# Kernel tuning notes

Measured on AMD Instinct MI355X. Metric: run time of the kernel, lower is better.

The kernel has to match this reference:

```python
import jax, jax.numpy as jnp
import numpy as np

BN_EPS = 1e-5


def ball_query(pos, radius, k):
    """PointNet++-style ball query: for each point, the first k point indices
    (in index order) whose distance < radius; shorter lists are padded with the
    first valid index (self is always valid since dist=0). pos: (b,n,3).
    Returns idx: (b,n,k) int32."""
    b, n, _ = pos.shape
    sq = jnp.sum(pos * pos, axis=-1)                       # (b,n)
    d2 = sq[:, :, None] + sq[:, None, :] - 2.0 * jnp.einsum('bnc,bmc->bnm', pos, pos)
    mask = d2 < radius * radius                            # (b,n,n)
    cand = jnp.where(mask, jnp.arange(n, dtype=jnp.int32)[None, None, :], jnp.int32(n))
    # smallest-k indices in ascending order == first-k valid in index order
    neg_top, _ = jax.lax.top_k(-cand, k)                   # (b,n,k)
    idx = -neg_top
    first = idx[..., :1]
    idx = jnp.where(idx == n, first, idx)                  # pad with first neighbor
    return idx


def reference(pos, x, w1, gamma, beta, w2, b2, radius, k):
    pos = jax.lax.stop_gradient(pos)
    idx = ball_query(pos, radius, k)                       # (b,n,k)
    grouped = jax.vmap(lambda p, i: p[i])(pos, idx)        # (b,n,k,3)
    rel = grouped - pos[:, :, None, :]                     # center-subtract
    # 1x1 conv (3->3, no bias)
    h = jnp.einsum('bnkc,dc->bnkd', rel, w1)
    # BatchNorm2d (training-mode batch stats over b,k,n per channel)
    mean = jnp.mean(h, axis=(0, 1, 2))
    var = jnp.mean((h - mean) ** 2, axis=(0, 1, 2))
    h = (h - mean) * jax.lax.rsqrt(var + BN_EPS) * gamma + beta
    h = jax.nn.relu(h)
    # 1x1 conv (3->out_channel) + bias
    pe = jnp.einsum('bnkd,ed->bnke', h, w2) + b2           # (b,n,k,C)
    pe = jnp.max(pe, axis=2)                               # max over k neighbors
    return x + pe


def setup_inputs() -> dict:
    key = jax.random.key(0)
    ks = jax.random.split(key, 5)
    b, n, c, kk = 2, 8192, 64, 32
    pos = jax.random.uniform(ks[0], (b, n, 3), dtype=jnp.float32)
    x = jax.random.normal(ks[1], (b, n, c), dtype=jnp.float32)
    w1 = jax.random.normal(ks[2], (3, 3), dtype=jnp.float32) * 0.5
    gamma = jnp.ones((3,), dtype=jnp.float32)
    beta = jnp.zeros((3,), dtype=jnp.float32)
    w2 = jax.random.normal(ks[3], (c, 3), dtype=jnp.float32) * 0.5
    b2 = jnp.zeros((c,), dtype=jnp.float32)
    radius = jnp.float32(0.1)
    return {"pos": pos, "x": x, "w1": w1, "gamma": gamma, "beta": beta,
            "w2": w2, "b2": b2, "radius": radius, "k": kk}
```

## Files before the change

kernel.cpp:

```cpp
#include <hip/hip_runtime.h>
#include <math.h>

#define NPTS   8192
#define NBATCH 2
#define NQ     (NPTS * NBATCH)
#define KNB    32
#define CFEAT  64
#define BN_EPS 1e-5f

#define MAXC     1000
#define CSTR     1024
#define CAP_HIT  128

#define QBK2  16
#define NBLK2 (NQ / QBK2)

#define QBK3  16
#define NBLK3 (NQ / QBK3)

#define WS_H     0
#define WS_PART  (WS_H + NQ * 3 * KNB)
#define WS_STATS (WS_PART + 6 * NBLK2)
#define WS_CS    (WS_STATS + 8)
#define WS_BIN   (WS_CS + 2 * CSTR)

__device__ __forceinline__ int grid_from_r(double rd) {
    int G = (int)(1.0 / rd);
    if (G < 1) G = 1;
    while (G > 1 && 1.0 / (double)G < rd) --G;
    if (G > 10) G = 10;
    return G;
}

__device__ __forceinline__ int mbcnt64(unsigned long long m) {
    return (int)__builtin_amdgcn_mbcnt_hi((unsigned)(m >> 32),
             __builtin_amdgcn_mbcnt_lo((unsigned)m, 0u));
}

__device__ __forceinline__ int cell_of(float v, float Gf, int G) {
    int c = (int)(v * Gf);
    return c > G - 1 ? G - 1 : c;
}

__global__ __launch_bounds__(1024) void kBin(
    const float* __restrict__ pos, const float* __restrict__ radius,
    float* __restrict__ ws)
{
    __shared__ int hist[MAXC];
    __shared__ int cur[MAXC];
    __shared__ int wtot[16];

    const int tid = threadIdx.x, lane = tid & 63, wave = tid >> 6;
    const int batch = blockIdx.x;

    const float* bpos = pos + (size_t)batch * NPTS * 3;
    const double rd = (double)radius[0];
    const int G = grid_from_r(rd);
    const float Gf = (float)G;
    const int NC = G * G * G;

    for (int c = tid; c < NC; c += 1024) hist[c] = 0;
    __syncthreads();

    for (int p = tid; p < NPTS; p += 1024) {
        const float* pp = bpos + (size_t)p * 3;
        int c = (cell_of(pp[2], Gf, G) * G + cell_of(pp[1], Gf, G)) * G
                + cell_of(pp[0], Gf, G);
        atomicAdd(&hist[c], 1);
    }
    __syncthreads();

    int v = (tid < NC) ? hist[tid] : 0;
    int incl = v;
#pragma unroll
    for (int off = 1; off < 64; off <<= 1) {
        int t = __shfl_up(incl, off);
        if (lane >= off) incl += t;
    }
    if (lane == 63) wtot[wave] = incl;
    __syncthreads();
    int base = 0;
#pragma unroll
    for (int w = 0; w < 16; ++w) base += (w < wave) ? wtot[w] : 0;
    const int excl = base + incl - v;
    int* cs = (int*)ws + WS_CS + batch * CSTR;
    if (tid < NC) { cs[tid] = excl; cur[tid] = excl; }
    if (tid == 0) cs[NC] = NPTS;
    __syncthreads();

    float4* bin = (float4*)(ws + WS_BIN) + (size_t)batch * NPTS;
    for (int p = tid; p < NPTS; p += 1024) {
        const float* pp = bpos + (size_t)p * 3;
        float x = pp[0], y = pp[1], z = pp[2];
        int c = (cell_of(z, Gf, G) * G + cell_of(y, Gf, G)) * G
                + cell_of(x, Gf, G);
        int slot = atomicAdd(&cur[c], 1);
        bin[slot] = make_float4(x, y, z, __int_as_float(p));
    }
}

__global__ __launch_bounds__(1024) void k2_query(
    const float* __restrict__ pos, const float* __restrict__ w1,
    const float* __restrict__ radius, float* __restrict__ ws)
{
    __shared__ int   hitl[QBK2][CAP_HIT];
    __shared__ int   seli[QBK2][KNB];
    __shared__ float sred[QBK2][6];

    const int tid = threadIdx.x, lane = tid & 63, wave = tid >> 6;
    const int qbase = blockIdx.x * QBK2;
    const int batch = qbase / NPTS;
    const float* bpos = pos + (size_t)batch * NPTS * 3;
    const double rd  = (double)radius[0];
    const double r2d = rd * rd;
    const int G = grid_from_r(rd);
    const float Gf = (float)G;
    const int* cs = (const int*)ws + WS_CS + batch * CSTR;
    const float4* bin = (const float4*)(ws + WS_BIN) + (size_t)batch * NPTS;

    const int qg = qbase + wave;
    const int ql = qg - batch * NPTS;
    const float qx = bpos[ql * 3], qy = bpos[ql * 3 + 1], qz = bpos[ql * 3 + 2];
    const double qxd = (double)qx, qyd = (double)qy, qzd = (double)qz;
    const double qsd = fma(qzd, qzd, fma(qyd, qyd, qxd * qxd));
    const int cx = cell_of(qx, Gf, G);
    const int cy = cell_of(qy, Gf, G);
    const int cz = cell_of(qz, Gf, G);
    const int cx0 = max(cx - 1, 0), cx1 = min(cx + 1, G - 1);

    int rs0[9], rpref[10];
    int tot = 0;
#pragma unroll
    for (int r = 0; r < 9; ++r) {
        const int ny = cy + (r % 3) - 1;
        const int nz = cz + (r / 3) - 1;
        int s0 = 0, len = 0;
        if (ny >= 0 && ny < G && nz >= 0 && nz < G) {
            const int cb = (nz * G + ny) * G;
            s0  = cs[cb + cx0];
            len = cs[cb + cx1 + 1] - s0;
        }
        rs0[r] = s0; rpref[r] = tot; tot += len;
    }
    rpref[9] = tot;

    int hc = 0;
    for (int b0 = 0; b0 < tot; b0 += 64) {
        const int flat = b0 + lane;
        const bool act = flat < tot;
        int ss = flat + (rs0[0] - rpref[0]);
#pragma unroll
        for (int i = 1; i < 9; ++i)
            ss += (flat >= rpref[i]) ? ((rs0[i] - rpref[i]) -
                                        (rs0[i - 1] - rpref[i - 1])) : 0;
        float4 P = bin[act ? ss : 0];
        double xj = (double)P.x, yj = (double)P.y, zj = (double)P.z;
        double sqj = fma(zj, zj, fma(yj, yj, xj * xj));
        double dot = fma(zj, qzd, fma(yj, qyd, xj * qxd));
        double dd  = (qsd + sqj) - 2.0 * dot;
        bool in = act && (dd < r2d);
        unsigned long long bal = __ballot(in);
        if (in) {
            int p2 = hc + mbcnt64(bal);
            if (p2 < CAP_HIT) hitl[wave][p2] = __float_as_int(P.w);
        }
        hc += (int)__popcll(bal);
    }
    if (hc > CAP_HIT) hc = CAP_HIT;

    if (hc <= KNB) {
        int v = (lane < hc) ? hitl[wave][lane] : 0x7FFFFFFF;
        int mn = v;
#pragma unroll
        for (int off = 32; off; off >>= 1) mn = min(mn, __shfl_xor(mn, off));
        if (lane < KNB) seli[wave][lane] = (lane < hc) ? v : mn;
    } else {
        int a = (lane < hc) ? hitl[wave][lane] : 0x7FFFFFFF;
        int b = (64 + lane < hc) ? hitl[wave][64 + lane] : 0x7FFFFFFF;
        int lo = 0, hi = NPTS - 1;
        while (lo < hi) {
            int mid = (lo + hi) >> 1;
            int c1 = (int)__popcll(__ballot(a <= mid)) +
                     (int)__popcll(__ballot(b <= mid));
            if (c1 >= KNB) hi = mid; else lo = mid + 1;
        }
        const int t = lo;
        unsigned long long ba = __ballot(a <= t);
        unsigned long long bb = __ballot(b <= t);
        int na = (int)__popcll(ba);
        if (a <= t) seli[wave][mbcnt64(ba)] = a;
        if (b <= t) seli[wave][na + mbcnt64(bb)] = b;
    }

    float w1r[9];
#pragma unroll
    for (int i = 0; i < 9; ++i) w1r[i] = w1[i];

    float ls0 = 0.f, ls1 = 0.f, ls2 = 0.f;
    float lq0 = 0.f, lq1 = 0.f, lq2 = 0.f;
    if (lane < KNB) {
        int j = seli[wave][lane];
        const float* pj = bpos + (size_t)j * 3;
        float rx = __fsub_rn(pj[0], qx);
        float ry = __fsub_rn(pj[1], qy);
        float rz = __fsub_rn(pj[2], qz);
        float h0 = fmaf(rz, w1r[2], fmaf(ry, w1r[1], __fmul_rn(rx, w1r[0])));
        float h1 = fmaf(rz, w1r[5], fmaf(ry, w1r[4], __fmul_rn(rx, w1r[3])));
        float h2 = fmaf(rz, w1r[8], fmaf(ry, w1r[7], __fmul_rn(rx, w1r[6])));
        float* hout = ws + WS_H + (size_t)qg * 3 * KNB;
        hout[0 * KNB + lane] = h0;
        hout[1 * KNB + lane] = h1;
        hout[2 * KNB + lane] = h2;
        ls0 = h0; ls1 = h1; ls2 = h2;
        lq0 = h0 * h0; lq1 = h1 * h1; lq2 = h2 * h2;
    }

#pragma unroll
    for (int m = 1; m < 64; m <<= 1) {
        ls0 += __shfl_xor(ls0, m); ls1 += __shfl_xor(ls1, m); ls2 += __shfl_xor(ls2, m);
        lq0 += __shfl_xor(lq0, m); lq1 += __shfl_xor(lq1, m); lq2 += __shfl_xor(lq2, m);
    }
    if (lane == 0) {
        sred[wave][0] = ls0; sred[wave][1] = ls1; sred[wave][2] = ls2;
        sred[wave][3] = lq0; sred[wave][4] = lq1; sred[wave][5] = lq2;
    }
    __syncthreads();
    if (tid < 6) {
        float s = 0.f;
#pragma unroll
        for (int w = 0; w < QBK2; ++w) s += sred[w][tid];
        ws[WS_PART + tid * NBLK2 + blockIdx.x] = s;
    }
}

__global__ __launch_bounds__(1024) void k2b_stats(float* __restrict__ ws)
{
    __shared__ float wred[16][6];
    const int tid = threadIdx.x, lane = tid & 63, wave = tid >> 6;

#pragma unroll
    for (int c = 0; c < 6; ++c) {
        float s = ws[WS_PART + c * NBLK2 + tid];
#pragma unroll
        for (int m = 1; m < 64; m <<= 1) s += __shfl_xor(s, m);
        if (lane == 0) wred[wave][c] = s;
    }
    __syncthreads();
    if (tid < 3) {
        const double N = (double)((long long)NQ * KNB);
        double s = 0.0, sq = 0.0;
#pragma unroll
        for (int w = 0; w < 16; ++w) { s += wred[w][tid]; sq += wred[w][3 + tid]; }
        double mean = s / N;
        double var  = sq / N - mean * mean;
        ws[WS_STATS + tid]     = (float)mean;
        ws[WS_STATS + 3 + tid] = (float)(1.0 / sqrt(var + (double)BN_EPS));
    }
}

__global__ __launch_bounds__(256) void k3_mlp(
    const float* __restrict__ ws, const float* __restrict__ gamma,
    const float* __restrict__ beta, const float* __restrict__ w2,
    const float* __restrict__ b2, const float* __restrict__ x,
    float* __restrict__ out)
{
    __shared__ float gl[QBK3 * 96];

    const int tid = threadIdx.x;
    const float m0 = ws[WS_STATS + 0], m1 = ws[WS_STATS + 1], m2 = ws[WS_STATS + 2];
    const float i0 = ws[WS_STATS + 3], i1 = ws[WS_STATS + 4], i2 = ws[WS_STATS + 5];
    const float g0 = gamma[0], g1 = gamma[1], g2 = gamma[2];
    const float b0 = beta[0],  b1 = beta[1],  b2c = beta[2];

    const int qbase = blockIdx.x * QBK3;
    const float* hin = ws + WS_H + (size_t)qbase * 96;

#pragma unroll
    for (int r = 0; r < 6; ++r) {
        const int idx = r * 256 + tid;
        const int c = (idx % 96) >> 5;
        float h = hin[idx];
        float mm = c == 0 ? m0 : (c == 1 ? m1 : m2);
        float ii = c == 0 ? i0 : (c == 1 ? i1 : i2);
        float gg = c == 0 ? g0 : (c == 1 ? g1 : g2);
        float bb = c == 0 ? b0 : (c == 1 ? b1 : b2c);
        float n = __fadd_rn(__fmul_rn(__fmul_rn(__fsub_rn(h, mm), ii), gg), bb);
        gl[idx] = fmaxf(n, 0.0f);
    }
    __syncthreads();

    const int ch = tid & 63;
    const int qh = tid >> 6;
    const float w20 = w2[ch * 3 + 0];
    const float w21 = w2[ch * 3 + 1];
    const float w22 = w2[ch * 3 + 2];
    const float bias = b2[ch];

#pragma unroll
    for (int r = 0; r < 4; ++r) {
        const int q = r * 4 + qh;
        const float* gq = &gl[q * 96];
        float m = -INFINITY;
#pragma unroll 4
        for (int kk = 0; kk < KNB; ++kk) {
            float ga = gq[kk], gb = gq[32 + kk], gc = gq[64 + kk];
            float pe = __fadd_rn(fmaf(gc, w22, fmaf(gb, w21, __fmul_rn(ga, w20))), bias);
            m = fmaxf(m, pe);
        }
        const size_t o = (size_t)(qbase + q) * CFEAT + ch;
        out[o] = __fadd_rn(x[o], m);
    }
}

extern "C" void kernel_launch(void* const* d_in, const int* in_sizes, int n_in,
                              void* d_out, int out_size, void* d_ws, size_t ws_size,
                              hipStream_t stream) {
    (void)in_sizes; (void)n_in; (void)out_size; (void)ws_size;
    const float* pos    = (const float*)d_in[0];
    const float* x      = (const float*)d_in[1];
    const float* w1     = (const float*)d_in[2];
    const float* gamma  = (const float*)d_in[3];
    const float* beta   = (const float*)d_in[4];
    const float* w2     = (const float*)d_in[5];
    const float* b2     = (const float*)d_in[6];
    const float* radius = (const float*)d_in[7];
    float* out = (float*)d_out;
    float* ws  = (float*)d_ws;

    hipLaunchKernelGGL(kBin,      dim3(NBATCH), dim3(1024), 0, stream, pos, radius, ws);
    hipLaunchKernelGGL(k2_query,  dim3(NBLK2),  dim3(1024), 0, stream, pos, w1, radius, ws);
    hipLaunchKernelGGL(k2b_stats, dim3(1),      dim3(1024), 0, stream, ws);
    hipLaunchKernelGGL(k3_mlp,    dim3(NBLK3),  dim3(256),  0, stream,
                       ws, gamma, beta, w2, b2, x, out);
}
```

Measured before the change: 56.87 us.

## Replace stats reduction kernel with fixed-point atomics and prefetch candidate loads

Drops the single-block BN statistics kernel. Each query block now adds its partial sums into 64-bit fixed-point accumulators with atomics, and the MLP kernel derives mean and inverse std from those accumulators itself, which removes one launch and one dependency gap. The candidate scan in the query kernel also software-pipelines the bin loads by prefetching the next 64-wide chunk while testing the current one. The fixed-point scaling adds a small quantization error to the statistics, and the accumulators are zeroed inside kBin, which relies on kernels running in stream order.

```diff
diff --git a/kernel.cpp b/kernel.cpp
--- a/kernel.cpp
+++ b/kernel.cpp
@@ -11,6 +11,7 @@
 #define MAXC     1000
 #define CSTR     1024
 #define CAP_HIT  128
+#define ACC_SCALE 16777216.0
 
 #define QBK2  16
 #define NBLK2 (NQ / QBK2)
@@ -19,9 +20,8 @@
 #define NBLK3 (NQ / QBK3)
 
 #define WS_H     0
-#define WS_PART  (WS_H + NQ * 3 * KNB)
-#define WS_STATS (WS_PART + 6 * NBLK2)
-#define WS_CS    (WS_STATS + 8)
+#define WS_ACC   (WS_H + NQ * 3 * KNB)
+#define WS_CS    (WS_ACC + 12)
 #define WS_BIN   (WS_CS + 2 * CSTR)
 
 __device__ __forceinline__ int grid_from_r(double rd) {
@@ -52,6 +52,8 @@
 
     const int tid = threadIdx.x, lane = tid & 63, wave = tid >> 6;
     const int batch = blockIdx.x;
+    if (batch == 0 && tid < 6)
+        ((long long*)(ws + WS_ACC))[tid] = 0LL;
 
     const float* bpos = pos + (size_t)batch * NPTS * 3;
     const double rd = (double)radius[0];
@@ -143,18 +145,34 @@
         rs0[r] = s0; rpref[r] = tot; tot += len;
     }
     rpref[9] = tot;
-
+    int del[9];
+#pragma unroll
+    for (int i = 0; i < 9; ++i) del[i] = rs0[i] - rpref[i];
+
+    const int nw = (tot + 63) >> 6;
     int hc = 0;
-    for (int b0 = 0; b0 < tot; b0 += 64) {
-        const int flat = b0 + lane;
+    float4 P;
+    {
+        const int flat = lane;
+        int ss = flat + del[0];
+#pragma unroll
+        for (int i = 1; i < 9; ++i)
+            ss += (flat >= rpref[i]) ? (del[i] - del[i - 1]) : 0;
+        P = bin[(flat < tot) ? ss : 0];
+    }
+    for (int w = 0; w < nw; ++w) {
+        const float4 Pc = P;
+        const int flat = (w << 6) + lane;
+        if (w + 1 < nw) {
+            const int fn = ((w + 1) << 6) + lane;
+            int ssn = fn + del[0];
+#pragma unroll
+            for (int i = 1; i < 9; ++i)
+                ssn += (fn >= rpref[i]) ? (del[i] - del[i - 1]) : 0;
+            P = bin[(fn < tot) ? ssn : 0];
+        }
         const bool act = flat < tot;
-        int ss = flat + (rs0[0] - rpref[0]);
-#pragma unroll
-        for (int i = 1; i < 9; ++i)
-            ss += (flat >= rpref[i]) ? ((rs0[i] - rpref[i]) -
-                                        (rs0[i - 1] - rpref[i - 1])) : 0;
-        float4 P = bin[act ? ss : 0];
-        double xj = (double)P.x, yj = (double)P.y, zj = (double)P.z;
+        double xj = (double)Pc.x, yj = (double)Pc.y, zj = (double)Pc.z;
         double sqj = fma(zj, zj, fma(yj, yj, xj * xj));
         double dot = fma(zj, qzd, fma(yj, qyd, xj * qxd));
         double dd  = (qsd + sqj) - 2.0 * dot;
@@ -162,7 +180,7 @@
         unsigned long long bal = __ballot(in);
         if (in) {
             int p2 = hc + mbcnt64(bal);
-            if (p2 < CAP_HIT) hitl[wave][p2] = __float_as_int(P.w);
+            if (p2 < CAP_HIT) hitl[wave][p2] = __float_as_int(Pc.w);
         }
         hc += (int)__popcll(bal);
     }
@@ -229,32 +247,9 @@
         float s = 0.f;
 #pragma unroll
         for (int w = 0; w < QBK2; ++w) s += sred[w][tid];
-        ws[WS_PART + tid * NBLK2 + blockIdx.x] = s;
-    }
-}
-
-__global__ __launch_bounds__(1024) void k2b_stats(float* __restrict__ ws)
-{
-    __shared__ float wred[16][6];
-    const int tid = threadIdx.x, lane = tid & 63, wave = tid >> 6;
-
-#pragma unroll
-    for (int c = 0; c < 6; ++c) {
-        float s = ws[WS_PART + c * NBLK2 + tid];
-#pragma unroll
-        for (int m = 1; m < 64; m <<= 1) s += __shfl_xor(s, m);
-        if (lane == 0) wred[wave][c] = s;
-    }
-    __syncthreads();
-    if (tid < 3) {
-        const double N = (double)((long long)NQ * KNB);
-        double s = 0.0, sq = 0.0;
-#pragma unroll
-        for (int w = 0; w < 16; ++w) { s += wred[w][tid]; sq += wred[w][3 + tid]; }
-        double mean = s / N;
-        double var  = sq / N - mean * mean;
-        ws[WS_STATS + tid]     = (float)mean;
-        ws[WS_STATS + 3 + tid] = (float)(1.0 / sqrt(var + (double)BN_EPS));
+        long long q = (long long)llrint((double)s * ACC_SCALE);
+        atomicAdd((unsigned long long*)(ws + WS_ACC) + tid,
+                  (unsigned long long)q);
     }
 }
 
@@ -267,8 +262,20 @@
     __shared__ float gl[QBK3 * 96];
 
     const int tid = threadIdx.x;
-    const float m0 = ws[WS_STATS + 0], m1 = ws[WS_STATS + 1], m2 = ws[WS_STATS + 2];
-    const float i0 = ws[WS_STATS + 3], i1 = ws[WS_STATS + 4], i2 = ws[WS_STATS + 5];
+    const long long* acc = (const long long*)(ws + WS_ACC);
+    const double N = (double)((long long)NQ * KNB);
+    float ms[3], is[3];
+#pragma unroll
+    for (int d = 0; d < 3; ++d) {
+        double s  = (double)acc[d]     / ACC_SCALE;
+        double sq = (double)acc[3 + d] / ACC_SCALE;
+        double mean = s / N;
+        double var  = sq / N - mean * mean;
+        ms[d] = (float)mean;
+        is[d] = (float)(1.0 / sqrt(var + (double)BN_EPS));
+    }
+    const float m0 = ms[0], m1 = ms[1], m2 = ms[2];
+    const float i0 = is[0], i1 = is[1], i2 = is[2];
     const float g0 = gamma[0], g1 = gamma[1], g2 = gamma[2];
     const float b0 = beta[0],  b1 = beta[1],  b2c = beta[2];
 
@@ -327,9 +334,8 @@
     float* out = (float*)d_out;
     float* ws  = (float*)d_ws;
 
-    hipLaunchKernelGGL(kBin,      dim3(NBATCH), dim3(1024), 0, stream, pos, radius, ws);
-    hipLaunchKernelGGL(k2_query,  dim3(NBLK2),  dim3(1024), 0, stream, pos, w1, radius, ws);
-    hipLaunchKernelGGL(k2b_stats, dim3(1),      dim3(1024), 0, stream, ws);
-    hipLaunchKernelGGL(k3_mlp,    dim3(NBLK3),  dim3(256),  0, stream,
+    hipLaunchKernelGGL(kBin,     dim3(NBATCH), dim3(1024), 0, stream, pos, radius, ws);
+    hipLaunchKernelGGL(k2_query, dim3(NBLK2),  dim3(1024), 0, stream, pos, w1, radius, ws);
+    hipLaunchKernelGGL(k3_mlp,   dim3(NBLK3),  dim3(256),  0, stream,
                        ws, gamma, beta, w2, b2, x, out);
 }
```

Result: no change. 56.13 us (median of 2 runs) (-1.3%).
